# Optimization experiments

Measured on AMD Instinct MI355X. Metric: run time of the kernel, lower is better.

Reference implementation:

```python
import jax, jax.numpy as jnp
import numpy as np

N_NODES = 100000
N_EDGES = 1600000
D_IN = 128
D_HID = 128
N_CLS = 16
N_GRAPHS = 64


def setup_inputs() -> dict:
    key = jax.random.key(0)
    ks = jax.random.split(key, 12)
    h = jax.random.normal(ks[0], (N_NODES, D_IN), dtype=jnp.float32)
    src = jax.random.randint(ks[1], (N_EDGES,), 0, N_NODES, dtype=jnp.int32)
    dst = jax.random.randint(ks[2], (N_EDGES,), 0, N_NODES, dtype=jnp.int32)
    graph_ids = jnp.sort(jax.random.randint(ks[3], (N_NODES,), 0, N_GRAPHS, dtype=jnp.int32))
    s = 1.0 / np.sqrt(D_IN)
    W1_self = jax.random.uniform(ks[4], (D_IN, D_HID), jnp.float32, -s, s)
    W1_neigh = jax.random.uniform(ks[5], (D_IN, D_HID), jnp.float32, -s, s)
    b1 = jnp.zeros((D_HID,), jnp.float32)
    s2 = 1.0 / np.sqrt(D_HID)
    W2_self = jax.random.uniform(ks[6], (D_HID, D_HID), jnp.float32, -s2, s2)
    W2_neigh = jax.random.uniform(ks[7], (D_HID, D_HID), jnp.float32, -s2, s2)
    b2 = jnp.zeros((D_HID,), jnp.float32)
    Wc = jax.random.uniform(ks[8], (D_HID, N_CLS), jnp.float32, -s2, s2)
    bc = jnp.zeros((N_CLS,), jnp.float32)
    return {"h": h, "src": src, "dst": dst, "graph_ids": graph_ids, "num_graphs": N_GRAPHS,
            "W1_self": W1_self, "W1_neigh": W1_neigh, "b1": b1,
            "W2_self": W2_self, "W2_neigh": W2_neigh, "b2": b2,
            "Wc": Wc, "bc": bc}


def _sage_conv(h, src, dst, W_self, W_neigh, b):
    # DGL SAGEConv 'mean': out = fc_self(h) + fc_neigh(mean of in-neighbor feats) + bias
    n = h.shape[0]
    msg = jnp.take(h, src, axis=0)                               # [E, d] gather
    agg = jax.ops.segment_sum(msg, dst, num_segments=n)          # [N, d] scatter-add
    deg = jax.ops.segment_sum(jnp.ones((src.shape[0],), h.dtype), dst, num_segments=n)
    neigh = agg / jnp.maximum(deg, 1.0)[:, None]                 # mean, zero-degree safe
    return h @ W_self + neigh @ W_neigh + b


def reference(h, src, dst, graph_ids, num_graphs,
              W1_self, W1_neigh, b1, W2_self, W2_neigh, b2, Wc, bc):
    x = jax.nn.relu(_sage_conv(h, src, dst, W1_self, W1_neigh, b1))
    x = _sage_conv(x, src, dst, W2_self, W2_neigh, b2)
    # dgl.mean_nodes: per-graph mean over node features
    gsum = jax.ops.segment_sum(x, graph_ids, num_segments=num_graphs)    # [G, d]
    gcnt = jax.ops.segment_sum(jnp.ones((x.shape[0],), x.dtype), graph_ids, num_segments=num_graphs)
    hg = gsum / jnp.maximum(gcnt, 1.0)[:, None]
    return hg @ Wc + bc                                                  # [G, num_classes]
```

## Files before the change

kernel.cpp:

```cpp
#include <hip/hip_runtime.h>

#define D        128
#define N_GRAPHS 64
#define N_CLS    16
#define LDA      40
#define SLOTS    48
#define CAP      8192

typedef unsigned int   uint;
typedef unsigned short ushort;
typedef __attribute__((ext_vector_type(8))) short short8;
typedef __attribute__((ext_vector_type(4))) float f32x4;

__device__ inline ushort f2b(float f) {
    uint u = __float_as_uint(f);
    u += 0x7fffu + ((u >> 16) & 1u);
    return (ushort)(u >> 16);
}

__device__ __forceinline__ int swz2i(int row, int col) {
    return row * 256 + (col ^ (((row ^ (row >> 3)) & 7) << 3));
}

#define ACC8(v)                                          \
    acc[0] += __uint_as_float((v).x << 16);              \
    acc[1] += __uint_as_float((v).x & 0xffff0000u);      \
    acc[2] += __uint_as_float((v).y << 16);              \
    acc[3] += __uint_as_float((v).y & 0xffff0000u);      \
    acc[4] += __uint_as_float((v).z << 16);              \
    acc[5] += __uint_as_float((v).z & 0xffff0000u);      \
    acc[6] += __uint_as_float((v).w << 16);              \
    acc[7] += __uint_as_float((v).w & 0xffff0000u);


__global__ __launch_bounds__(256) void k_boot(
    const float* __restrict__ h, ushort* __restrict__ fb,
    const float* __restrict__ Ws, const float* __restrict__ Wn,
    ushort* __restrict__ wT,
    const int* __restrict__ gid, int* __restrict__ gstart,
    const int* __restrict__ src, const int* __restrict__ dst,
    int* __restrict__ bcount, uint* __restrict__ ebuf,
    int* __restrict__ bcount2, uint* __restrict__ ebuf2, int doP2,
    int E, int NB, int N, int t4) {
    __shared__ int h1[512], b1s[512], c1[512];
    __shared__ int h2[512], b2s[512], c2[512];
    int bb = blockIdx.x;
    int t  = threadIdx.x;

    if (bb < 256) {
        int per = (E + 255) / 256;
        int e0 = bb * per;
        int e1 = min(e0 + per, E);
        for (int i = t; i < NB; i += 256) {
            h1[i] = 0; c1[i] = 0; h2[i] = 0; c2[i] = 0;
        }
        __syncthreads();
        for (int e = e0 + t; e < e1; e += 256) {
            atomicAdd(&h1[dst[e] >> 8], 1);
            if (doP2) atomicAdd(&h2[src[e] >> 8], 1);
        }
        __syncthreads();
        for (int i = t; i < NB; i += 256) {
            b1s[i] = h1[i] ? atomicAdd(&bcount[i], h1[i]) : 0;
            if (doP2) b2s[i] = h2[i] ? atomicAdd(&bcount2[i], h2[i]) : 0;
        }
        __syncthreads();
        for (int e = e0 + t; e < e1; e += 256) {
            int ss = src[e];
            int dd = dst[e];
            int bk1 = dd >> 8;
            int p1 = b1s[bk1] + atomicAdd(&c1[bk1], 1);
            if (p1 < CAP)
                ebuf[(size_t)bk1 * CAP + p1] = ((uint)ss << 8) | (uint)(dd & 255);
            if (doP2) {
                int bk2 = ss >> 8;
                int p2 = b2s[bk2] + atomicAdd(&c2[bk2], 1);
                if (p2 < CAP)
                    ebuf2[(size_t)bk2 * CAP + p2] = ((uint)dd << 8) | (uint)(ss & 255);
            }
        }
    } else if (bb < 384) {
        int i = (bb - 256) * 256 + t;
        int c = i >> 8, k = i & 255;
        float v = (k < 128) ? Ws[k * 128 + c] : Wn[(k - 128) * 128 + c];
        wT[c * 256 + k] = f2b(v);
    } else if (bb == 384) {
        int g = t;
        if (g <= N_GRAPHS) {
            int lo = 0, hi = N;
            while (lo < hi) {
                int mid = (lo + hi) >> 1;
                if (gid[mid] < g) lo = mid + 1; else hi = mid;
            }
            gstart[g] = lo;
        }
    } else {
        int i = (bb - 385) * 256 + t;
        if (i < t4) {
            float4 v = ((const float4*)h)[i];
            ushort4 o;
            o.x = f2b(v.x); o.y = f2b(v.y); o.z = f2b(v.z); o.w = f2b(v.w);
            ((ushort4*)fb)[i] = o;
        }
    }
}


__global__ __launch_bounds__(1024) void k_bucket(
    const uint* __restrict__ ebuf, const int* __restrict__ bcount,
    const int* __restrict__ gid,
    int* __restrict__ csrf, int* __restrict__ deg, float* __restrict__ invdeg,
    uint2* __restrict__ gipack, int N) {
    __shared__ int ldeg[256];
    __shared__ int lcsr[256 * SLOTS];
    int b = blockIdx.x, t = threadIdx.x;
    if (t < 256) ldeg[t] = 0;
    __syncthreads();
    int cnt = bcount[b];
    if (cnt > CAP) cnt = CAP;
    const uint* __restrict__ eb = ebuf + (size_t)b * CAP;
    for (int i = t; i < cnt; i += 1024) {
        uint r = eb[i];
        int dl = r & 255;
        int sl = atomicAdd(&ldeg[dl], 1);
        if (sl < SLOTS) lcsr[dl * SLOTS + sl] = (int)(r >> 8);
    }
    __syncthreads();
    int n0 = b << 8;
    int lim = (N - n0) * SLOTS;
    if (lim > 256 * SLOTS) lim = 256 * SLOTS;
    for (int i = t; i < lim; i += 1024)
        csrf[(size_t)n0 * SLOTS + i] = lcsr[i];
    if (t < 256 && n0 + t < N) {
        int d = ldeg[t];
        deg[n0 + t] = d;
        float iv = 1.0f / (float)(d > 1 ? d : 1);
        invdeg[n0 + t] = iv;
        gipack[n0 + t] = make_uint2((uint)gid[n0 + t], __float_as_uint(iv));
    }
}


__global__ __launch_bounds__(256) void k_aggb(
    const ushort* __restrict__ fb, const int* __restrict__ deg,
    const int* __restrict__ csrf, const float* __restrict__ invdeg,
    ushort* __restrict__ outb, int N) {
    int lane = threadIdx.x & 63;
    int n = blockIdx.x * 4 + (threadIdx.x >> 6);
    if (n >= N) return;
    int d = deg[n];
    if (d > SLOTS) d = SLOTS;
    const int* __restrict__ lst = csrf + (size_t)n * SLOTS;
    int ej = lane >> 4;
    int cg = lane & 15;

    float acc[8];
#pragma unroll
    for (int i = 0; i < 8; i++) acc[i] = 0.f;

    int e = ej;
    for (; e + 12 < d; e += 16) {
        int s0 = lst[e];
        int s1 = lst[e + 4];
        int s2 = lst[e + 8];
        int s3 = lst[e + 12];
        uint4 v0 = *(const uint4*)(fb + (size_t)s0 * D + cg * 8);
        uint4 v1 = *(const uint4*)(fb + (size_t)s1 * D + cg * 8);
        uint4 v2 = *(const uint4*)(fb + (size_t)s2 * D + cg * 8);
        uint4 v3 = *(const uint4*)(fb + (size_t)s3 * D + cg * 8);
        ACC8(v0); ACC8(v1); ACC8(v2); ACC8(v3);
    }
    for (; e + 4 < d; e += 8) {
        int s0 = lst[e];
        int s1 = lst[e + 4];
        uint4 v0 = *(const uint4*)(fb + (size_t)s0 * D + cg * 8);
        uint4 v1 = *(const uint4*)(fb + (size_t)s1 * D + cg * 8);
        ACC8(v0); ACC8(v1);
    }
    for (; e < d; e += 4) {
        int s = lst[e];
        uint4 v = *(const uint4*)(fb + (size_t)s * D + cg * 8);
        ACC8(v);
    }
#pragma unroll
    for (int i = 0; i < 8; i++) {
        acc[i] += __shfl_xor(acc[i], 16);
        acc[i] += __shfl_xor(acc[i], 32);
    }
    if (ej == 0) {
        float id = invdeg[n];
        uint4 o;
        o.x = (uint)f2b(acc[0] * id) | ((uint)f2b(acc[1] * id) << 16);
        o.y = (uint)f2b(acc[2] * id) | ((uint)f2b(acc[3] * id) << 16);
        o.z = (uint)f2b(acc[4] * id) | ((uint)f2b(acc[5] * id) << 16);
        o.w = (uint)f2b(acc[6] * id) | ((uint)f2b(acc[7] * id) << 16);
        *(uint4*)(outb + (size_t)n * D + cg * 8) = o;
    }
}

__global__ __launch_bounds__(256) void k_part2s(
    const int* __restrict__ src, const int* __restrict__ dst,
    int* __restrict__ bcount2, uint* __restrict__ ebuf2, int E, int NB) {
    __shared__ int hist[512], base[512], lcur[512];
    int t = threadIdx.x;
    int per = (E + 255) / 256;
    int e0 = blockIdx.x * per;
    int e1 = min(e0 + per, E);
    for (int i = t; i < NB; i += 256) { hist[i] = 0; lcur[i] = 0; }
    __syncthreads();
    for (int e = e0 + t; e < e1; e += 256) atomicAdd(&hist[src[e] >> 8], 1);
    __syncthreads();
    for (int i = t; i < NB; i += 256)
        base[i] = hist[i] ? atomicAdd(&bcount2[i], hist[i]) : 0;
    __syncthreads();
    for (int e = e0 + t; e < e1; e += 256) {
        int ss = src[e];
        int bk = ss >> 8;
        int off = atomicAdd(&lcur[bk], 1);
        int pos = base[bk] + off;
        if (pos < CAP)
            ebuf2[(size_t)bk * CAP + pos] = ((uint)dst[e] << 8) | (uint)(ss & 255);
    }
}


__global__ __launch_bounds__(256, 2) void k_mm1m(
    const ushort* __restrict__ hb, const ushort* __restrict__ nbb,
    const ushort* __restrict__ wT, const float* __restrict__ b,
    const int* __restrict__ gid, float* __restrict__ S1,
    ushort* __restrict__ x1b, int N) {
    __shared__ __align__(16) ushort As[128 * LDA];
    __shared__ __align__(16) ushort Bs[128 * LDA];
    __shared__ float s1l[2][128];
    int t    = threadIdx.x;
    int w    = t >> 6;
    int lane = t & 63;
    int m    = lane & 15;
    int quad = lane >> 4;
    int n0   = blockIdx.x * 128;

    ((float*)s1l)[t] = 0.f;
    if (t < 256) ((float*)s1l)[t + 256 < 512 ? t + 256 : t] = 0.f;

    f32x4 acc[2][8];
#pragma unroll
    for (int rt = 0; rt < 2; rt++)
#pragma unroll
        for (int ct = 0; ct < 8; ct++) acc[rt][ct] = (f32x4){0.f, 0.f, 0.f, 0.f};

#pragma unroll 1
    for (int kc = 0; kc < 8; kc++) {
        int k0 = kc * 32;
        const ushort* __restrict__ A = (k0 < 128) ? hb : nbb;
        int ka = k0 & 127;
        __syncthreads();
#pragma unroll
        for (int i = 0; i < 2; i++) {
            int linear = i * 256 + t;
            int row = linear >> 2;
            int q   = linear & 3;
            int nn = n0 + row;
            uint4 v = make_uint4(0u, 0u, 0u, 0u);
            if (nn < N) v = *(const uint4*)(A + (size_t)nn * D + ka + q * 8);
            *(uint4*)(&As[row * LDA + q * 8]) = v;
        }
#pragma unroll
        for (int i = 0; i < 2; i++) {
            int linear = i * 256 + t;
            int col = linear >> 2;
            int q   = linear & 3;
            uint4 v = *(const uint4*)(wT + (size_t)col * 256 + k0 + q * 8);
            *(uint4*)(&Bs[col * LDA + q * 8]) = v;
        }
        __syncthreads();
        short8 af[2], bf[8];
#pragma unroll
        for (int rt = 0; rt < 2; rt++)
            af[rt] = *(const short8*)(&As[(w * 32 + rt * 16 + m) * LDA + quad * 8]);
#pragma unroll
        for (int ct = 0; ct < 8; ct++)
            bf[ct] = *(const short8*)(&Bs[(ct * 16 + m) * LDA + quad * 8]);
#pragma unroll
        for (int rt = 0; rt < 2; rt++)
#pragma unroll
            for (int ct = 0; ct < 8; ct++)
                acc[rt][ct] = __builtin_amdgcn_mfma_f32_16x16x32_bf16(
                    af[rt], bf[ct], acc[rt][ct], 0, 0, 0);
    }

    int g0 = gid[n0];
    int gofs[2][4];
#pragma unroll
    for (int rt = 0; rt < 2; rt++)
#pragma unroll
        for (int r = 0; r < 4; r++) {
            int n = n0 + w * 32 + rt * 16 + quad * 4 + r;
            gofs[rt][r] = (n < N) ? (gid[n] - g0) : -1;
        }

#pragma unroll
    for (int ct = 0; ct < 8; ct++) {
        float bias = b[ct * 16 + m];
        float vlo = 0.f, vhi = 0.f;
#pragma unroll
        for (int rt = 0; rt < 2; rt++) {
#pragma unroll
            for (int r = 0; r < 4; r++) {
                int go = gofs[rt][r];
                if (go < 0) continue;
                int n = n0 + w * 32 + rt * 16 + quad * 4 + r;
                float v = fmaxf(acc[rt][ct][r] + bias, 0.f);
                x1b[(size_t)n * D + ct * 16 + m] = f2b(v);
                if (go == 0) vlo += v;
                else if (go == 1) vhi += v;
                else atomicAdd(&S1[(g0 + go) * D + ct * 16 + m], v);
            }
        }
        vlo += __shfl_xor(vlo, 16); vlo += __shfl_xor(vlo, 32);
        vhi += __shfl_xor(vhi, 16); vhi += __shfl_xor(vhi, 32);
        if (quad == 0) {
            if (vlo != 0.f) atomicAdd(&s1l[0][ct * 16 + m], vlo);
            if (vhi != 0.f) atomicAdd(&s1l[1][ct * 16 + m], vhi);
        }
    }
    __syncthreads();
    if (t < 256) {
        int g = t >> 7, c = t & 127;
        float v = s1l[g][c];
        if (v != 0.f && g0 + g < N_GRAPHS) atomicAdd(&S1[(g0 + g) * D + c], v);
    }
}


__global__ __launch_bounds__(1024, 4) void k_wg(
    const uint* __restrict__ ebuf2, const int* __restrict__ bcount2,
    const uint2* __restrict__ gipack,
    const ushort* __restrict__ x1b, float* __restrict__ P, int N) {
    __shared__ __align__(16) char smem[131072];
    float*  lwcT = (float*)smem;
    ushort* lxT  = (ushort*)smem;
    ushort* lwcb = (ushort*)(smem + 65536);
    ushort* lwlo = (ushort*)(smem + 98304);

    int b = blockIdx.x, t = threadIdx.x;
    int n0 = b << 8;

    for (int i = t; i < 16384; i += 1024) lwcT[i] = 0.f;
    __syncthreads();

    int cnt = bcount2[b];
    if (cnt > CAP) cnt = CAP;
    const uint* __restrict__ eb = ebuf2 + (size_t)b * CAP;
    for (int i = t; i < cnt; i += 1024) {
        uint r = eb[i];
        int dn = (int)(r >> 8);
        int sl = (int)(r & 255u);
        uint2 gi = gipack[dn];
        atomicAdd(&lwcT[gi.x * 256 + sl], __uint_as_float(gi.y));
    }
    __syncthreads();

    for (int i = t; i < 16384; i += 1024) {
        int g = i >> 8, sl = i & 255;
        float v = lwcT[i];
        ushort hi = f2b(v);
        float fhi = __uint_as_float((uint)hi << 16);
        ushort lo = f2b(v - fhi);
        int si = swz2i(g, sl);
        lwcb[si] = hi;
        lwlo[si] = lo;
    }
    __syncthreads();

    const uint4* __restrict__ x4 = (const uint4*)x1b;
#pragma unroll 1
    for (int it = 0; it < 4; ++it) {
        int l = it * 1024 + t;
        int n = l >> 4, q = l & 15;
        uint4 v = make_uint4(0u, 0u, 0u, 0u);
        int nn = n0 + n;
        if (nn < N) v = x4[(size_t)nn * 16 + q];
        int d0 = q * 8;
        lxT[swz2i(d0 + 0, n)] = (ushort)(v.x & 0xffffu);
        lxT[swz2i(d0 + 1, n)] = (ushort)(v.x >> 16);
        lxT[swz2i(d0 + 2, n)] = (ushort)(v.y & 0xffffu);
        lxT[swz2i(d0 + 3, n)] = (ushort)(v.y >> 16);
        lxT[swz2i(d0 + 4, n)] = (ushort)(v.z & 0xffffu);
        lxT[swz2i(d0 + 5, n)] = (ushort)(v.z >> 16);
        lxT[swz2i(d0 + 6, n)] = (ushort)(v.w & 0xffffu);
        lxT[swz2i(d0 + 7, n)] = (ushort)(v.w >> 16);
    }
    __syncthreads();

    int wv = t >> 6, lane = t & 63, m = lane & 15, quad = lane >> 4;
    int s  = wv & 3;
    int hs = wv >> 2;
    f32x4 acc[2];
    acc[0] = (f32x4){0.f, 0.f, 0.f, 0.f};
    acc[1] = (f32x4){0.f, 0.f, 0.f, 0.f};

#pragma unroll 1
    for (int k8 = 0; k8 < 8; ++k8) {
        int kc = k8 * 32 + quad * 8;
        int ar = s * 16 + m;
        short8 ahi = *(const short8*)&lwcb[swz2i(ar, kc)];
        short8 alo = *(const short8*)&lwlo[swz2i(ar, kc)];
#pragma unroll
        for (int d2 = 0; d2 < 2; ++d2) {
            short8 bfr = *(const short8*)&lxT[swz2i(hs * 32 + d2 * 16 + m, kc)];
            acc[d2] = __builtin_amdgcn_mfma_f32_16x16x32_bf16(alo, bfr, acc[d2], 0, 0, 0);
            acc[d2] = __builtin_amdgcn_mfma_f32_16x16x32_bf16(ahi, bfr, acc[d2], 0, 0, 0);
        }
    }
    float* __restrict__ Pb = P + (size_t)b * 8192;
#pragma unroll
    for (int d2 = 0; d2 < 2; ++d2) {
#pragma unroll
        for (int r = 0; r < 4; ++r) {
            int g = s * 16 + quad * 4 + r;
            Pb[g * 128 + hs * 32 + d2 * 16 + m] = acc[d2][r];
        }
    }
}


__global__ __launch_bounds__(256) void k_final(
    const float* __restrict__ S1, const float* __restrict__ P, int NBLK,
    const int* __restrict__ gstart, const float* __restrict__ W2s,
    const float* __restrict__ W2n, const float* __restrict__ b2,
    const float* __restrict__ Wc, const float* __restrict__ bc,
    float* __restrict__ out) {
    __shared__ float s1[D], s2[2][D], hg[D];
    int g = blockIdx.x, t = threadIdx.x;
    int c = t & 127, hh = t >> 7;
    const float* __restrict__ Pg = P + (size_t)g * 128 + c;
    float a0 = 0.f, a1 = 0.f, a2 = 0.f, a3 = 0.f;
    int bb = hh;
    for (; bb + 6 < NBLK; bb += 8) {
        a0 += Pg[(size_t)bb * 8192];
        a1 += Pg[(size_t)(bb + 2) * 8192];
        a2 += Pg[(size_t)(bb + 4) * 8192];
        a3 += Pg[(size_t)(bb + 6) * 8192];
    }
    for (; bb < NBLK; bb += 2) a0 += Pg[(size_t)bb * 8192];
    s2[hh][c] = a0 + a1 + a2 + a3;
    if (hh == 0) s1[c] = S1[g * D + c];
    __syncthreads();
    if (t < 128) s2[0][c] += s2[1][c];
    __syncthreads();
    if (t < 128) {
        float acc = 0.f;
#pragma unroll 8
        for (int k = 0; k < D; k++) {
            acc = fmaf(s1[k], W2s[k * D + c], acc);
            acc = fmaf(s2[0][k], W2n[k * D + c], acc);
        }
        int cnt = gstart[g + 1] - gstart[g];
        hg[c] = (cnt > 0) ? (acc / (float)cnt + b2[c]) : 0.f;
    }
    __syncthreads();
    if (t < N_CLS) {
        float o = bc[t];
        for (int k = 0; k < D; k++) o = fmaf(hg[k], Wc[k * N_CLS + t], o);
        out[g * N_CLS + t] = o;
    }
}


extern "C" void kernel_launch(void* const* d_in, const int* in_sizes, int n_in,
                              void* d_out, int out_size, void* d_ws, size_t ws_size,
                              hipStream_t stream) {
    const float* h   = (const float*)d_in[0];
    const int*   src = (const int*)d_in[1];
    const int*   dst = (const int*)d_in[2];
    const int*   gid = (const int*)d_in[3];
    const float* W1s = (const float*)d_in[5];
    const float* W1n = (const float*)d_in[6];
    const float* b1  = (const float*)d_in[7];
    const float* W2s = (const float*)d_in[8];
    const float* W2n = (const float*)d_in[9];
    const float* b2  = (const float*)d_in[10];
    const float* Wc  = (const float*)d_in[11];
    const float* bc  = (const float*)d_in[12];
    float* out = (float*)d_out;

    const int N = in_sizes[0] / D;
    const int E = in_sizes[1];
    const int NB = (N + 255) >> 8;

    char* w = (char*)d_ws;
    size_t off = 0;
    auto alloc = [&](size_t elems) -> void* {
        void* p = w + off;
        off += elems * 4;
        return p;
    };
    float* S1      = (float*)alloc((size_t)N_GRAPHS * D);
    int*   bcount  = (int*)alloc(512);
    int*   bcount2 = (int*)alloc(512);
    size_t zero_bytes = off;
    int*   deg    = (int*)alloc(N);
    float* invdeg = (float*)alloc(N);
    uint2* gipack = (uint2*)alloc((size_t)N * 2);
    int*   gstart = (int*)alloc(128);
    int*   csrf   = (int*)alloc((size_t)N * SLOTS);
    ushort* fb    = (ushort*)alloc((size_t)N * 64);
    ushort* nbb   = (ushort*)alloc((size_t)N * 64);
    ushort* x1b   = (ushort*)alloc((size_t)N * 64);
    ushort* wT    = (ushort*)alloc(16384);
    uint*  ebuf = (uint*)nbb;
    float* P    = (float*)fb;

    size_t ebuf2_units = (size_t)NB * CAP;
    bool dedicated = (off + ebuf2_units * 4) <= ws_size;
    uint* ebuf2 = dedicated ? (uint*)alloc(ebuf2_units) : (uint*)csrf;

    hipMemsetAsync(d_ws, 0, zero_bytes, stream);

    int t4 = N * 32;
    int CB = (t4 + 255) / 256;
    int MMB = (N + 127) / 128;
    int AB  = (N + 3) / 4;

    k_boot<<<385 + CB, 256, 0, stream>>>(
        h, fb, W1s, W1n, wT, gid, gstart, src, dst,
        bcount, ebuf, bcount2, ebuf2, dedicated ? 1 : 0, E, NB, N, t4);
    k_bucket<<<NB, 1024, 0, stream>>>(ebuf, bcount, gid, csrf, deg, invdeg, gipack, N);
    k_aggb<<<AB, 256, 0, stream>>>(fb, deg, csrf, invdeg, nbb, N);
    if (!dedicated)
        k_part2s<<<256, 256, 0, stream>>>(src, dst, bcount2, ebuf2, E, NB);
    k_mm1m<<<MMB, 256, 0, stream>>>(fb, nbb, wT, b1, gid, S1, x1b, N);
    k_wg<<<NB, 1024, 0, stream>>>(ebuf2, bcount2, gipack, x1b, P, N);
    k_final<<<N_GRAPHS, 256, 0, stream>>>(
        S1, P, NB, gstart, W2s, W2n, b2, Wc, bc, out);
}
```

Measured before the change: 315.1 us.

## Halve k_wg source-bucket size and split edge partitioning into separate boot blocks

Source buckets for the second-layer weighted-graph step shrink from 256 to 128 nodes. k_wg now runs with 512 threads and 48KB of LDS instead of 1024 threads and 128KB, so more blocks fit per CU. The x1 tile is staged in two 64-node chunks, and each wave computes four MMA column tiles. The dst and src edge partitioning in k_boot moves to separate block ranges so both run in parallel, not fused per block. The cost is twice as many partial P blocks for k_final to reduce and a smaller per-bucket capacity (4096), which could overflow on skewed inputs.

Result: slower. 333.6 us (+5.9%).

```diff
diff --git a/kernel.cpp b/kernel.cpp
--- a/kernel.cpp
+++ b/kernel.cpp
@@ -6,6 +6,7 @@
 #define LDA      40
 #define SLOTS    48
 #define CAP      8192
+#define CAP2     4096
 
 typedef unsigned int   uint;
 typedef unsigned short ushort;
@@ -18,8 +19,11 @@
     return (ushort)(u >> 16);
 }
 
-__device__ __forceinline__ int swz2i(int row, int col) {
-    return row * 256 + (col ^ (((row ^ (row >> 3)) & 7) << 3));
+__device__ __forceinline__ int aswz(int g, int c) {
+    return g * 128 + (c ^ ((g & 15) << 3));
+}
+__device__ __forceinline__ int bswz(int d, int c) {
+    return d * 64 + (c ^ ((d & 7) << 3));
 }
 
 #define ACC8(v)                                          \
@@ -41,9 +45,8 @@
     const int* __restrict__ src, const int* __restrict__ dst,
     int* __restrict__ bcount, uint* __restrict__ ebuf,
     int* __restrict__ bcount2, uint* __restrict__ ebuf2, int doP2,
-    int E, int NB, int N, int t4) {
-    __shared__ int h1[512], b1s[512], c1[512];
-    __shared__ int h2[512], b2s[512], c2[512];
+    int E, int NB, int NB2, int N, int t4) {
+    __shared__ int hist[1024], base[1024], lcur[1024];
     int bb = blockIdx.x;
     int t  = threadIdx.x;
 
@@ -51,40 +54,48 @@
         int per = (E + 255) / 256;
         int e0 = bb * per;
         int e1 = min(e0 + per, E);
-        for (int i = t; i < NB; i += 256) {
-            h1[i] = 0; c1[i] = 0; h2[i] = 0; c2[i] = 0;
-        }
+        for (int i = t; i < NB; i += 256) { hist[i] = 0; lcur[i] = 0; }
+        __syncthreads();
+        for (int e = e0 + t; e < e1; e += 256) atomicAdd(&hist[dst[e] >> 8], 1);
+        __syncthreads();
+        for (int i = t; i < NB; i += 256)
+            base[i] = hist[i] ? atomicAdd(&bcount[i], hist[i]) : 0;
         __syncthreads();
         for (int e = e0 + t; e < e1; e += 256) {
-            atomicAdd(&h1[dst[e] >> 8], 1);
-            if (doP2) atomicAdd(&h2[src[e] >> 8], 1);
-        }
-        __syncthreads();
-        for (int i = t; i < NB; i += 256) {
-            b1s[i] = h1[i] ? atomicAdd(&bcount[i], h1[i]) : 0;
-            if (doP2) b2s[i] = h2[i] ? atomicAdd(&bcount2[i], h2[i]) : 0;
-        }
+            int dd = dst[e];
+            int b = dd >> 8;
+            int off = atomicAdd(&lcur[b], 1);
+            int pos = base[b] + off;
+            if (pos < CAP)
+                ebuf[(size_t)b * CAP + pos] = ((uint)src[e] << 8) | (uint)(dd & 255);
+        }
+    } else if (bb < 512) {
+        if (!doP2) return;
+        int bb2 = bb - 256;
+        int per = (E + 255) / 256;
+        int e0 = bb2 * per;
+        int e1 = min(e0 + per, E);
+        for (int i = t; i < NB2; i += 256) { hist[i] = 0; lcur[i] = 0; }
+        __syncthreads();
+        for (int e = e0 + t; e < e1; e += 256) atomicAdd(&hist[src[e] >> 7], 1);
+        __syncthreads();
+        for (int i = t; i < NB2; i += 256)
+            base[i] = hist[i] ? atomicAdd(&bcount2[i], hist[i]) : 0;
         __syncthreads();
         for (int e = e0 + t; e < e1; e += 256) {
             int ss = src[e];
-            int dd = dst[e];
-            int bk1 = dd >> 8;
-            int p1 = b1s[bk1] + atomicAdd(&c1[bk1], 1);
-            if (p1 < CAP)
-                ebuf[(size_t)bk1 * CAP + p1] = ((uint)ss << 8) | (uint)(dd & 255);
-            if (doP2) {
-                int bk2 = ss >> 8;
-                int p2 = b2s[bk2] + atomicAdd(&c2[bk2], 1);
-                if (p2 < CAP)
-                    ebuf2[(size_t)bk2 * CAP + p2] = ((uint)dd << 8) | (uint)(ss & 255);
-            }
-        }
-    } else if (bb < 384) {
-        int i = (bb - 256) * 256 + t;
+            int bk = ss >> 7;
+            int off = atomicAdd(&lcur[bk], 1);
+            int pos = base[bk] + off;
+            if (pos < CAP2)
+                ebuf2[(size_t)bk * CAP2 + pos] = ((uint)dst[e] << 7) | (uint)(ss & 127);
+        }
+    } else if (bb < 640) {
+        int i = (bb - 512) * 256 + t;
         int c = i >> 8, k = i & 255;
         float v = (k < 128) ? Ws[k * 128 + c] : Wn[(k - 128) * 128 + c];
         wT[c * 256 + k] = f2b(v);
-    } else if (bb == 384) {
+    } else if (bb == 640) {
         int g = t;
         if (g <= N_GRAPHS) {
             int lo = 0, hi = N;
@@ -95,7 +106,7 @@
             gstart[g] = lo;
         }
     } else {
-        int i = (bb - 385) * 256 + t;
+        int i = (bb - 641) * 256 + t;
         if (i < t4) {
             float4 v = ((const float4*)h)[i];
             ushort4 o;
@@ -200,26 +211,26 @@
 
 __global__ __launch_bounds__(256) void k_part2s(
     const int* __restrict__ src, const int* __restrict__ dst,
-    int* __restrict__ bcount2, uint* __restrict__ ebuf2, int E, int NB) {
-    __shared__ int hist[512], base[512], lcur[512];
+    int* __restrict__ bcount2, uint* __restrict__ ebuf2, int E, int NB2) {
+    __shared__ int hist[1024], base[1024], lcur[1024];
     int t = threadIdx.x;
     int per = (E + 255) / 256;
     int e0 = blockIdx.x * per;
     int e1 = min(e0 + per, E);
-    for (int i = t; i < NB; i += 256) { hist[i] = 0; lcur[i] = 0; }
-    __syncthreads();
-    for (int e = e0 + t; e < e1; e += 256) atomicAdd(&hist[src[e] >> 8], 1);
-    __syncthreads();
-    for (int i = t; i < NB; i += 256)
+    for (int i = t; i < NB2; i += 256) { hist[i] = 0; lcur[i] = 0; }
+    __syncthreads();
+    for (int e = e0 + t; e < e1; e += 256) atomicAdd(&hist[src[e] >> 7], 1);
+    __syncthreads();
+    for (int i = t; i < NB2; i += 256)
         base[i] = hist[i] ? atomicAdd(&bcount2[i], hist[i]) : 0;
     __syncthreads();
     for (int e = e0 + t; e < e1; e += 256) {
         int ss = src[e];
-        int bk = ss >> 8;
+        int bk = ss >> 7;
         int off = atomicAdd(&lcur[bk], 1);
         int pos = base[bk] + off;
-        if (pos < CAP)
-            ebuf2[(size_t)bk * CAP + pos] = ((uint)dst[e] << 8) | (uint)(ss & 255);
+        if (pos < CAP2)
+            ebuf2[(size_t)bk * CAP2 + pos] = ((uint)dst[e] << 7) | (uint)(ss & 127);
     }
 }
 
@@ -240,7 +251,7 @@
     int n0   = blockIdx.x * 128;
 
     ((float*)s1l)[t] = 0.f;
-    if (t < 256) ((float*)s1l)[t + 256 < 512 ? t + 256 : t] = 0.f;
+    ((float*)s1l)[t + 256] = 0.f;
 
     f32x4 acc[2][8];
 #pragma unroll
@@ -332,93 +343,100 @@
 }
 
 
-__global__ __launch_bounds__(1024, 4) void k_wg(
+__global__ __launch_bounds__(512, 6) void k_wg(
     const uint* __restrict__ ebuf2, const int* __restrict__ bcount2,
     const uint2* __restrict__ gipack,
     const ushort* __restrict__ x1b, float* __restrict__ P, int N) {
-    __shared__ __align__(16) char smem[131072];
+    __shared__ __align__(16) char smem[49152];
     float*  lwcT = (float*)smem;
-    ushort* lxT  = (ushort*)smem;
-    ushort* lwcb = (ushort*)(smem + 65536);
-    ushort* lwlo = (ushort*)(smem + 98304);
+    ushort* lhi  = (ushort*)smem;
+    ushort* llo  = (ushort*)(smem + 16384);
+    ushort* lxT  = (ushort*)(smem + 32768);
 
     int b = blockIdx.x, t = threadIdx.x;
-    int n0 = b << 8;
-
-    for (int i = t; i < 16384; i += 1024) lwcT[i] = 0.f;
+    int n0 = b << 7;
+
+    for (int i = t; i < 8192; i += 512) lwcT[i] = 0.f;
     __syncthreads();
 
     int cnt = bcount2[b];
-    if (cnt > CAP) cnt = CAP;
-    const uint* __restrict__ eb = ebuf2 + (size_t)b * CAP;
-    for (int i = t; i < cnt; i += 1024) {
+    if (cnt > CAP2) cnt = CAP2;
+    const uint* __restrict__ eb = ebuf2 + (size_t)b * CAP2;
+    for (int i = t; i < cnt; i += 512) {
         uint r = eb[i];
-        int dn = (int)(r >> 8);
-        int sl = (int)(r & 255u);
+        int dn = (int)(r >> 7);
+        int sl = (int)(r & 127u);
         uint2 gi = gipack[dn];
-        atomicAdd(&lwcT[gi.x * 256 + sl], __uint_as_float(gi.y));
-    }
-    __syncthreads();
-
-    for (int i = t; i < 16384; i += 1024) {
-        int g = i >> 8, sl = i & 255;
-        float v = lwcT[i];
-        ushort hi = f2b(v);
+        atomicAdd(&lwcT[gi.x * 128 + sl], __uint_as_float(gi.y));
+    }
+    __syncthreads();
+
+    float v[16];
+#pragma unroll
+    for (int j = 0; j < 16; j++) v[j] = lwcT[t * 16 + j];
+    __syncthreads();
+#pragma unroll
+    for (int j = 0; j < 16; j++) {
+        int i = t * 16 + j;
+        int g = i >> 7, sl = i & 127;
+        ushort hi = f2b(v[j]);
         float fhi = __uint_as_float((uint)hi << 16);
-        ushort lo = f2b(v - fhi);
-        int si = swz2i(g, sl);
-        lwcb[si] = hi;
-        lwlo[si] = lo;
-    }
-    __syncthreads();
-
-    const uint4* __restrict__ x4 = (const uint4*)x1b;
-#pragma unroll 1
-    for (int it = 0; it < 4; ++it) {
-        int l = it * 1024 + t;
-        int n = l >> 4, q = l & 15;
-        uint4 v = make_uint4(0u, 0u, 0u, 0u);
-        int nn = n0 + n;
-        if (nn < N) v = x4[(size_t)nn * 16 + q];
-        int d0 = q * 8;
-        lxT[swz2i(d0 + 0, n)] = (ushort)(v.x & 0xffffu);
-        lxT[swz2i(d0 + 1, n)] = (ushort)(v.x >> 16);
-        lxT[swz2i(d0 + 2, n)] = (ushort)(v.y & 0xffffu);
-        lxT[swz2i(d0 + 3, n)] = (ushort)(v.y >> 16);
-        lxT[swz2i(d0 + 4, n)] = (ushort)(v.z & 0xffffu);
-        lxT[swz2i(d0 + 5, n)] = (ushort)(v.z >> 16);
-        lxT[swz2i(d0 + 6, n)] = (ushort)(v.w & 0xffffu);
-        lxT[swz2i(d0 + 7, n)] = (ushort)(v.w >> 16);
-    }
-    __syncthreads();
+        ushort lo = f2b(v[j] - fhi);
+        int ai = aswz(g, sl);
+        lhi[ai] = hi;
+        llo[ai] = lo;
+    }
 
     int wv = t >> 6, lane = t & 63, m = lane & 15, quad = lane >> 4;
     int s  = wv & 3;
     int hs = wv >> 2;
-    f32x4 acc[2];
-    acc[0] = (f32x4){0.f, 0.f, 0.f, 0.f};
-    acc[1] = (f32x4){0.f, 0.f, 0.f, 0.f};
-
+    f32x4 acc[4];
+#pragma unroll
+    for (int d2 = 0; d2 < 4; ++d2) acc[d2] = (f32x4){0.f, 0.f, 0.f, 0.f};
+
+    const uint4* __restrict__ x4 = (const uint4*)x1b;
 #pragma unroll 1
-    for (int k8 = 0; k8 < 8; ++k8) {
-        int kc = k8 * 32 + quad * 8;
-        int ar = s * 16 + m;
-        short8 ahi = *(const short8*)&lwcb[swz2i(ar, kc)];
-        short8 alo = *(const short8*)&lwlo[swz2i(ar, kc)];
-#pragma unroll
-        for (int d2 = 0; d2 < 2; ++d2) {
-            short8 bfr = *(const short8*)&lxT[swz2i(hs * 32 + d2 * 16 + m, kc)];
-            acc[d2] = __builtin_amdgcn_mfma_f32_16x16x32_bf16(alo, bfr, acc[d2], 0, 0, 0);
-            acc[d2] = __builtin_amdgcn_mfma_f32_16x16x32_bf16(ahi, bfr, acc[d2], 0, 0, 0);
+    for (int ck = 0; ck < 2; ++ck) {
+        __syncthreads();
+        for (int l = t; l < 1024; l += 512) {
+            int n = l >> 4, q = l & 15;
+            int nn = n0 + ck * 64 + n;
+            uint4 vv = make_uint4(0u, 0u, 0u, 0u);
+            if (nn < N) vv = x4[(size_t)nn * 16 + q];
+            int d0 = q * 8;
+            lxT[bswz(d0 + 0, n)] = (ushort)(vv.x & 0xffffu);
+            lxT[bswz(d0 + 1, n)] = (ushort)(vv.x >> 16);
+            lxT[bswz(d0 + 2, n)] = (ushort)(vv.y & 0xffffu);
+            lxT[bswz(d0 + 3, n)] = (ushort)(vv.y >> 16);
+            lxT[bswz(d0 + 4, n)] = (ushort)(vv.z & 0xffffu);
+            lxT[bswz(d0 + 5, n)] = (ushort)(vv.z >> 16);
+            lxT[bswz(d0 + 6, n)] = (ushort)(vv.w & 0xffffu);
+            lxT[bswz(d0 + 7, n)] = (ushort)(vv.w >> 16);
+        }
+        __syncthreads();
+#pragma unroll
+        for (int k8 = 0; k8 < 2; ++k8) {
+            int ar = s * 16 + m;
+            int ka = ck * 64 + k8 * 32 + quad * 8;
+            short8 ahi = *(const short8*)&lhi[aswz(ar, ka)];
+            short8 alo = *(const short8*)&llo[aswz(ar, ka)];
+            int kb = k8 * 32 + quad * 8;
+#pragma unroll
+            for (int d2 = 0; d2 < 4; ++d2) {
+                int dr = hs * 64 + d2 * 16 + m;
+                short8 bfr = *(const short8*)&lxT[bswz(dr, kb)];
+                acc[d2] = __builtin_amdgcn_mfma_f32_16x16x32_bf16(alo, bfr, acc[d2], 0, 0, 0);
+                acc[d2] = __builtin_amdgcn_mfma_f32_16x16x32_bf16(ahi, bfr, acc[d2], 0, 0, 0);
+            }
         }
     }
     float* __restrict__ Pb = P + (size_t)b * 8192;
 #pragma unroll
-    for (int d2 = 0; d2 < 2; ++d2) {
+    for (int d2 = 0; d2 < 4; ++d2) {
 #pragma unroll
         for (int r = 0; r < 4; ++r) {
             int g = s * 16 + quad * 4 + r;
-            Pb[g * 128 + hs * 32 + d2 * 16 + m] = acc[d2][r];
+            Pb[g * 128 + hs * 64 + d2 * 16 + m] = acc[d2][r];
         }
     }
 }
@@ -486,7 +504,8 @@
 
     const int N = in_sizes[0] / D;
     const int E = in_sizes[1];
-    const int NB = (N + 255) >> 8;
+    const int NB  = (N + 255) >> 8;
+    const int NB2 = (N + 127) >> 7;
 
     char* w = (char*)d_ws;
     size_t off = 0;
@@ -497,7 +516,7 @@
     };
     float* S1      = (float*)alloc((size_t)N_GRAPHS * D);
     int*   bcount  = (int*)alloc(512);
-    int*   bcount2 = (int*)alloc(512);
+    int*   bcount2 = (int*)alloc(1024);
     size_t zero_bytes = off;
     int*   deg    = (int*)alloc(N);
     float* invdeg = (float*)alloc(N);
@@ -511,7 +530,7 @@
     uint*  ebuf = (uint*)nbb;
     float* P    = (float*)fb;
 
-    size_t ebuf2_units = (size_t)NB * CAP;
+    size_t ebuf2_units = (size_t)NB2 * CAP2;
     bool dedicated = (off + ebuf2_units * 4) <= ws_size;
     uint* ebuf2 = dedicated ? (uint*)alloc(ebuf2_units) : (uint*)csrf;
 
@@ -522,15 +541,15 @@
     int MMB = (N + 127) / 128;
     int AB  = (N + 3) / 4;
 
-    k_boot<<<385 + CB, 256, 0, stream>>>(
+    k_boot<<<641 + CB, 256, 0, stream>>>(
         h, fb, W1s, W1n, wT, gid, gstart, src, dst,
-        bcount, ebuf, bcount2, ebuf2, dedicated ? 1 : 0, E, NB, N, t4);
+        bcount, ebuf, bcount2, ebuf2, dedicated ? 1 : 0, E, NB, NB2, N, t4);
     k_bucket<<<NB, 1024, 0, stream>>>(ebuf, bcount, gid, csrf, deg, invdeg, gipack, N);
     k_aggb<<<AB, 256, 0, stream>>>(fb, deg, csrf, invdeg, nbb, N);
     if (!dedicated)
-        k_part2s<<<256, 256, 0, stream>>>(src, dst, bcount2, ebuf2, E, NB);
+        k_part2s<<<256, 256, 0, stream>>>(src, dst, bcount2, ebuf2, E, NB2);
     k_mm1m<<<MMB, 256, 0, stream>>>(fb, nbb, wT, b1, gid, S1, x1b, N);
-    k_wg<<<NB, 1024, 0, stream>>>(ebuf2, bcount2, gipack, x1b, P, N);
+    k_wg<<<NB2, 512, 0, stream>>>(ebuf2, bcount2, gipack, x1b, P, N);
     k_final<<<N_GRAPHS, 256, 0, stream>>>(
-        S1, P, NB, gstart, W2s, W2n, b2, Wc, bc, out);
-}
+        S1, P, NB2, gstart, W2s, W2n, b2, Wc, bc, out);
+}
```

## Split edge partition passes into separate blocks and move bf16 conversion into bucket kernel

Applied to the files above, without the earlier changes.

The boot kernel now runs the dst-keyed and src-keyed edge partitions in separate block ranges (256 blocks each) instead of one block doing both, which halves per-block serial work and shared-memory histogram footprint. The fp32-to-bf16 feature conversion moves out of k_boot into the bucket kernel as extra 1024-thread blocks, so it overlaps with CSR bucketing. A redundant shared-memory zeroing and a guard in k_mm1m are removed. Edges are read twice from global memory, and the bucket kernel's large LDS allocation now also applies to the conversion blocks, which may reduce their occupancy.

After: 314.7 us. No clear change (-0.1%).

```diff
diff --git a/kernel.cpp b/kernel.cpp
--- a/kernel.cpp
+++ b/kernel.cpp
@@ -34,16 +34,14 @@
 
 
 __global__ __launch_bounds__(256) void k_boot(
-    const float* __restrict__ h, ushort* __restrict__ fb,
     const float* __restrict__ Ws, const float* __restrict__ Wn,
     ushort* __restrict__ wT,
     const int* __restrict__ gid, int* __restrict__ gstart,
     const int* __restrict__ src, const int* __restrict__ dst,
     int* __restrict__ bcount, uint* __restrict__ ebuf,
     int* __restrict__ bcount2, uint* __restrict__ ebuf2, int doP2,
-    int E, int NB, int N, int t4) {
-    __shared__ int h1[512], b1s[512], c1[512];
-    __shared__ int h2[512], b2s[512], c2[512];
+    int E, int NB, int N) {
+    __shared__ int hist[512], base[512], lcur[512];
     int bb = blockIdx.x;
     int t  = threadIdx.x;
 
@@ -51,40 +49,48 @@
         int per = (E + 255) / 256;
         int e0 = bb * per;
         int e1 = min(e0 + per, E);
-        for (int i = t; i < NB; i += 256) {
-            h1[i] = 0; c1[i] = 0; h2[i] = 0; c2[i] = 0;
-        }
+        for (int i = t; i < NB; i += 256) { hist[i] = 0; lcur[i] = 0; }
+        __syncthreads();
+        for (int e = e0 + t; e < e1; e += 256) atomicAdd(&hist[dst[e] >> 8], 1);
+        __syncthreads();
+        for (int i = t; i < NB; i += 256)
+            base[i] = hist[i] ? atomicAdd(&bcount[i], hist[i]) : 0;
         __syncthreads();
         for (int e = e0 + t; e < e1; e += 256) {
-            atomicAdd(&h1[dst[e] >> 8], 1);
-            if (doP2) atomicAdd(&h2[src[e] >> 8], 1);
-        }
-        __syncthreads();
-        for (int i = t; i < NB; i += 256) {
-            b1s[i] = h1[i] ? atomicAdd(&bcount[i], h1[i]) : 0;
-            if (doP2) b2s[i] = h2[i] ? atomicAdd(&bcount2[i], h2[i]) : 0;
-        }
+            int dd = dst[e];
+            int b = dd >> 8;
+            int off = atomicAdd(&lcur[b], 1);
+            int pos = base[b] + off;
+            if (pos < CAP)
+                ebuf[(size_t)b * CAP + pos] = ((uint)src[e] << 8) | (uint)(dd & 255);
+        }
+    } else if (bb < 512) {
+        if (!doP2) return;
+        int bb2 = bb - 256;
+        int per = (E + 255) / 256;
+        int e0 = bb2 * per;
+        int e1 = min(e0 + per, E);
+        for (int i = t; i < NB; i += 256) { hist[i] = 0; lcur[i] = 0; }
+        __syncthreads();
+        for (int e = e0 + t; e < e1; e += 256) atomicAdd(&hist[src[e] >> 8], 1);
+        __syncthreads();
+        for (int i = t; i < NB; i += 256)
+            base[i] = hist[i] ? atomicAdd(&bcount2[i], hist[i]) : 0;
         __syncthreads();
         for (int e = e0 + t; e < e1; e += 256) {
             int ss = src[e];
-            int dd = dst[e];
-            int bk1 = dd >> 8;
-            int p1 = b1s[bk1] + atomicAdd(&c1[bk1], 1);
-            if (p1 < CAP)
-                ebuf[(size_t)bk1 * CAP + p1] = ((uint)ss << 8) | (uint)(dd & 255);
-            if (doP2) {
-                int bk2 = ss >> 8;
-                int p2 = b2s[bk2] + atomicAdd(&c2[bk2], 1);
-                if (p2 < CAP)
-                    ebuf2[(size_t)bk2 * CAP + p2] = ((uint)dd << 8) | (uint)(ss & 255);
-            }
-        }
-    } else if (bb < 384) {
-        int i = (bb - 256) * 256 + t;
+            int bk = ss >> 8;
+            int off = atomicAdd(&lcur[bk], 1);
+            int pos = base[bk] + off;
+            if (pos < CAP)
+                ebuf2[(size_t)bk * CAP + pos] = ((uint)dst[e] << 8) | (uint)(ss & 255);
+        }
+    } else if (bb < 640) {
+        int i = (bb - 512) * 256 + t;
         int c = i >> 8, k = i & 255;
         float v = (k < 128) ? Ws[k * 128 + c] : Wn[(k - 128) * 128 + c];
         wT[c * 256 + k] = f2b(v);
-    } else if (bb == 384) {
+    } else {
         int g = t;
         if (g <= N_GRAPHS) {
             int lo = 0, hi = N;
@@ -94,26 +100,33 @@
             }
             gstart[g] = lo;
         }
-    } else {
-        int i = (bb - 385) * 256 + t;
+    }
+}
+
+
+__global__ __launch_bounds__(1024) void k_bc(
+    const uint* __restrict__ ebuf, const int* __restrict__ bcount,
+    const int* __restrict__ gid,
+    int* __restrict__ csrf, int* __restrict__ deg, float* __restrict__ invdeg,
+    uint2* __restrict__ gipack,
+    const float* __restrict__ h, ushort* __restrict__ fb,
+    int N, int NB, int t4) {
+    __shared__ int ldeg[256];
+    __shared__ int lcsr[256 * SLOTS];
+    int t = threadIdx.x;
+
+    if (blockIdx.x >= NB) {
+        int i = (blockIdx.x - NB) * 1024 + t;
         if (i < t4) {
             float4 v = ((const float4*)h)[i];
             ushort4 o;
             o.x = f2b(v.x); o.y = f2b(v.y); o.z = f2b(v.z); o.w = f2b(v.w);
             ((ushort4*)fb)[i] = o;
         }
-    }
-}
-
-
-__global__ __launch_bounds__(1024) void k_bucket(
-    const uint* __restrict__ ebuf, const int* __restrict__ bcount,
-    const int* __restrict__ gid,
-    int* __restrict__ csrf, int* __restrict__ deg, float* __restrict__ invdeg,
-    uint2* __restrict__ gipack, int N) {
-    __shared__ int ldeg[256];
-    __shared__ int lcsr[256 * SLOTS];
-    int b = blockIdx.x, t = threadIdx.x;
+        return;
+    }
+
+    int b = blockIdx.x;
     if (t < 256) ldeg[t] = 0;
     __syncthreads();
     int cnt = bcount[b];
@@ -240,7 +253,6 @@
     int n0   = blockIdx.x * 128;
 
     ((float*)s1l)[t] = 0.f;
-    if (t < 256) ((float*)s1l)[t + 256 < 512 ? t + 256 : t] = 0.f;
 
     f32x4 acc[2][8];
 #pragma unroll
@@ -324,7 +336,7 @@
         }
     }
     __syncthreads();
-    if (t < 256) {
+    {
         int g = t >> 7, c = t & 127;
         float v = s1l[g][c];
         if (v != 0.f && g0 + g < N_GRAPHS) atomicAdd(&S1[(g0 + g) * D + c], v);
@@ -518,14 +530,15 @@
     hipMemsetAsync(d_ws, 0, zero_bytes, stream);
 
     int t4 = N * 32;
-    int CB = (t4 + 255) / 256;
+    int CB = (t4 + 1023) / 1024;
     int MMB = (N + 127) / 128;
     int AB  = (N + 3) / 4;
 
-    k_boot<<<385 + CB, 256, 0, stream>>>(
-        h, fb, W1s, W1n, wT, gid, gstart, src, dst,
-        bcount, ebuf, bcount2, ebuf2, dedicated ? 1 : 0, E, NB, N, t4);
-    k_bucket<<<NB, 1024, 0, stream>>>(ebuf, bcount, gid, csrf, deg, invdeg, gipack, N);
+    k_boot<<<641, 256, 0, stream>>>(
+        W1s, W1n, wT, gid, gstart, src, dst,
+        bcount, ebuf, bcount2, ebuf2, dedicated ? 1 : 0, E, NB, N);
+    k_bc<<<NB + CB, 1024, 0, stream>>>(
+        ebuf, bcount, gid, csrf, deg, invdeg, gipack, h, fb, N, NB, t4);
     k_aggb<<<AB, 256, 0, stream>>>(fb, deg, csrf, invdeg, nbb, N);
     if (!dedicated)
         k_part2s<<<256, 256, 0, stream>>>(src, dst, bcount2, ebuf2, E, NB);
```
